# Kernel tuning notes

Hardware: AMD Instinct MI355X
Metric: run time of the kernel (lower is better)

## Reference

```python
import math
import jax, jax.numpy as jnp
import numpy as np

L, D, H, F, V, S = 4, 1024, 16, 4096, 50257, 2048
HS = D // H
EPS = 1e-5
STD = 0.02


def setup_inputs() -> dict:
    key = jax.random.key(0)
    keys = iter(jax.random.split(key, 24))

    def rn(shape):
        return (jax.random.normal(next(keys), shape, jnp.float32) * STD)

    inp = {
        "input_ids": jax.random.randint(next(keys), (1, S), 0, V, dtype=jnp.int64),
        "tok_emb": rn((V, D)),
        "pos_emb": rn((S, D)),
        # per-layer stacked params; linear weights stored [in, out]
        "Wq": rn((L, D, D)), "bq": jnp.zeros((L, D)),
        "Wk": rn((L, D, D)), "bk": jnp.zeros((L, D)),
        "Wv": rn((L, D, D)), "bv": jnp.zeros((L, D)),
        "Wo": rn((L, D, D)), "bo": jnp.zeros((L, D)),
        "W1": rn((L, D, F)), "b1": jnp.zeros((L, F)),
        "W2": rn((L, F, D)), "b2": jnp.zeros((L, D)),
        "ln1w": jnp.ones((L, D)), "ln1b": jnp.zeros((L, D)),
        "ln2w": jnp.ones((L, D)), "ln2b": jnp.zeros((L, D)),
        "lnfw": jnp.ones((D,)), "lnfb": jnp.zeros((D,)),
        "lm_head": rn((V, D)),  # torch Linear weight layout [out, in]
    }
    return inp


def _layernorm(x, w, b):
    m = jnp.mean(x, axis=-1, keepdims=True)
    v = jnp.mean(jnp.square(x - m), axis=-1, keepdims=True)
    return (x - m) * jax.lax.rsqrt(v + EPS) * w + b


def reference(input_ids, tok_emb, pos_emb, Wq, bq, Wk, bk, Wv, bv, Wo, bo,
              W1, b1, W2, b2, ln1w, ln1b, ln2w, ln2b, lnfw, lnfb, lm_head):
    B, Sq = input_ids.shape
    h = tok_emb[input_ids] + pos_emb[None, :Sq]  # [B,S,D]
    causal = jnp.tril(jnp.ones((Sq, Sq), dtype=bool))
    scale = 1.0 / math.sqrt(HS)

    def block(h, p):
        wq, bq_, wk, bk_, wv, bv_, wo, bo_, w1, b1_, w2, b2_, l1w, l1b, l2w, l2b = p
        x = _layernorm(h, l1w, l1b)
        q = (x @ wq + bq_).reshape(B, Sq, H, HS).transpose(0, 2, 1, 3)
        k = (x @ wk + bk_).reshape(B, Sq, H, HS).transpose(0, 2, 1, 3)
        v = (x @ wv + bv_).reshape(B, Sq, H, HS).transpose(0, 2, 1, 3)
        scores = jnp.einsum('bhqd,bhkd->bhqk', q, k) * scale
        scores = jnp.where(causal, scores, jnp.finfo(scores.dtype).min)
        attn = jax.nn.softmax(scores, axis=-1)  # dropout is identity at eval
        out = jnp.einsum('bhqk,bhkd->bhqd', attn, v)
        out = out.transpose(0, 2, 1, 3).reshape(B, Sq, D)
        h = h + out @ wo + bo_
        x = _layernorm(h, l2w, l2b)
        h = h + jax.nn.gelu(x @ w1 + b1_, approximate=False) @ w2 + b2_
        return h, None

    h, _ = jax.lax.scan(block, h, (Wq, bq, Wk, bk, Wv, bv, Wo, bo,
                                   W1, b1, W2, b2, ln1w, ln1b, ln2w, ln2b))
    h = _layernorm(h, lnfw, lnfb)
    logits = h @ lm_head.T  # [B,S,V]
    return logits
```

## Files before the change

kernel.cpp:

```cpp
#include <hip/hip_runtime.h>
#include <math.h>
#include <stdint.h>


#define SEQ 2048
#define DIM 1024
#define NHEAD 16
#define FFN 4096
#define VOCAB 50257
#define NLAYER 4
#define LNEPS 1e-5f
#define QKVD 3072
#define KVB 128

using bf16x8 = __attribute__((ext_vector_type(8))) short;
using s16x4  = __attribute__((ext_vector_type(4))) short;
using f32x4  = __attribute__((ext_vector_type(4))) float;
using fl4    = __attribute__((ext_vector_type(4))) float;

static __device__ __forceinline__ short f2bf(float f) {
  uint32_t u = __float_as_uint(f);
  u = (u + 0x7fffu + ((u >> 16) & 1u)) >> 16;
  return (short)u;
}
static __device__ __forceinline__ float bf2f(short s) {
  return __uint_as_float(((uint32_t)(uint16_t)s) << 16);
}
static __device__ __forceinline__ void gload_lds16(const void* g, void* l) {
  __builtin_amdgcn_global_load_lds((const __attribute__((address_space(1))) void*)g,
                                   (__attribute__((address_space(3))) void*)l, 16, 0, 0);
}

__global__ void embed_kernel(const int* __restrict__ ids,
                             const float* __restrict__ tok,
                             const float* __restrict__ pos,
                             float* __restrict__ h) {
  int i = blockIdx.x * blockDim.x + threadIdx.x;
  if (i < SEQ * DIM) {
    int s = i / DIM, d = i % DIM;
    h[i] = tok[(long)ids[s] * DIM + d] + pos[i];
  }
}

__global__ void ln_kernel(const float* __restrict__ x, const float* __restrict__ w,
                          const float* __restrict__ b, short* __restrict__ y) {
  int row = blockIdx.x;
  const float* xr = x + (long)row * DIM;
  short* yr = y + (long)row * DIM;
  int tid = threadIdx.x;
  float v0 = xr[tid], v1 = xr[tid + 256], v2 = xr[tid + 512], v3 = xr[tid + 768];
  __shared__ float red[8];
  float s = v0 + v1 + v2 + v3;
#pragma unroll
  for (int o = 32; o >= 1; o >>= 1) s += __shfl_xor(s, o);
  if ((tid & 63) == 0) red[tid >> 6] = s;
  __syncthreads();
  float mean = (red[0] + red[1] + red[2] + red[3]) * (1.f / DIM);
  float d0 = v0 - mean, d1 = v1 - mean, d2 = v2 - mean, d3 = v3 - mean;
  float q = d0 * d0 + d1 * d1 + d2 * d2 + d3 * d3;
#pragma unroll
  for (int o = 32; o >= 1; o >>= 1) q += __shfl_xor(q, o);
  if ((tid & 63) == 0) red[4 + (tid >> 6)] = q;
  __syncthreads();
  float var = (red[4] + red[5] + red[6] + red[7]) * (1.f / DIM);
  float rstd = rsqrtf(var + LNEPS);
  yr[tid]       = f2bf(d0 * rstd * w[tid] + b[tid]);
  yr[tid + 256] = f2bf(d1 * rstd * w[tid + 256] + b[tid + 256]);
  yr[tid + 512] = f2bf(d2 * rstd * w[tid + 512] + b[tid + 512]);
  yr[tid + 768] = f2bf(d3 * rstd * w[tid + 768] + b[tid + 768]);
}

__global__ void transpose_w(const float* __restrict__ in, short* __restrict__ out,
                            int K, int N) {
  __shared__ float t[32][33];
  int c0 = blockIdx.x * 32, r0 = blockIdx.y * 32;
  int tx = threadIdx.x & 31, ty = threadIdx.x >> 5;
#pragma unroll
  for (int i = 0; i < 4; i++)
    t[ty + i * 8][tx] = in[(long)(r0 + ty + i * 8) * N + c0 + tx];
  __syncthreads();
#pragma unroll
  for (int i = 0; i < 4; i++)
    out[(long)(c0 + ty + i * 8) * K + r0 + tx] = f2bf(t[tx][ty + i * 8]);
}

struct TW4 { const float* src[4]; short* dst[4]; };
__global__ void transpose_w4(TW4 p) {
  const float* in = p.src[blockIdx.z];
  short* out = p.dst[blockIdx.z];
  __shared__ float t[32][33];
  int c0 = blockIdx.x * 32, r0 = blockIdx.y * 32;
  int tx = threadIdx.x & 31, ty = threadIdx.x >> 5;
#pragma unroll
  for (int i = 0; i < 4; i++)
    t[ty + i * 8][tx] = in[(long)(r0 + ty + i * 8) * DIM + c0 + tx];
  __syncthreads();
#pragma unroll
  for (int i = 0; i < 4; i++)
    out[(long)(c0 + ty + i * 8) * DIM + r0 + tx] = f2bf(t[tx][ty + i * 8]);
}

__global__ void transpose_v(const short* __restrict__ qkv, short* __restrict__ vt) {
  __shared__ short t[64][72];
  int s0 = blockIdx.x * 64, c0 = blockIdx.y * 64;
  int tid = threadIdx.x;
#pragma unroll
  for (int i = 0; i < 2; i++) {
    int ca = i * 256 + tid;
    int row = ca >> 3, cp = ca & 7;
    bf16x8 v = *(const bf16x8*)(qkv + (long)(s0 + row) * QKVD + 2 * DIM + c0 + cp * 8);
    *(bf16x8*)&t[row][cp * 8] = v;
  }
  __syncthreads();
#pragma unroll
  for (int i = 0; i < 2; i++) {
    int ca = i * 256 + tid;
    int crow = ca >> 3, sp = ca & 7;
    s16x4 a, b;
#pragma unroll
    for (int u = 0; u < 4; u++) a[u] = t[sp * 8 + u][crow];
#pragma unroll
    for (int u = 0; u < 4; u++) b[u] = t[sp * 8 + 4 + u][crow];
    bf16x8 o;
#pragma unroll
    for (int u = 0; u < 4; u++) { o[u] = a[u]; o[4 + u] = b[u]; }
    *(bf16x8*)(vt + (long)(c0 + crow) * SEQ + s0 + sp * 8) = o;
  }
}

__global__ void conv_bf16(const float* __restrict__ in, short* __restrict__ out, long n4) {
  long i = (long)blockIdx.x * blockDim.x + threadIdx.x;
  long stride = (long)gridDim.x * blockDim.x;
  for (; i < n4; i += stride) {
    fl4 v = *(const fl4*)(in + i * 4);
    s16x4 o;
    o[0] = f2bf(v[0]); o[1] = f2bf(v[1]); o[2] = f2bf(v[2]); o[3] = f2bf(v[3]);
    *(s16x4*)(out + i * 4) = o;
  }
}

__global__ void bias_cat(const float* __restrict__ bq, const float* __restrict__ bk,
                         const float* __restrict__ bv, float* __restrict__ out) {
  int i = blockIdx.x * 256 + threadIdx.x;
  if (i < QKVD) out[i] = i < DIM ? bq[i] : (i < 2 * DIM ? bk[i - DIM] : bv[i - 2 * DIM]);
}

template <bool GELU, bool RES, bool BIAS, bool OUTBF16, int KS, bool XCDSWZ>
__global__ __launch_bounds__(256, 3) void gemm4(
    const short* __restrict__ A, const short* __restrict__ Bt,
    const float* __restrict__ bias, const float* __restrict__ res,
    void* __restrict__ Cout, int N, int Kfull) {
  __shared__ short lds[3][(128 + 128) * 32];
  const int tid = threadIdx.x, wid = tid >> 6, lane = tid & 63;
  const int l16 = lane & 15, lg = lane >> 4;
  int bx = blockIdx.x, by = blockIdx.y;
  if (XCDSWZ) {
    int gx = gridDim.x, nwg = gx * gridDim.y;
    int flat = by * gx + bx;
    int nf = (flat & 7) * (nwg >> 3) + (flat >> 3);
    bx = nf % gx; by = nf / gx;
  }
  const long m0 = (long)bx * 128, n0 = (long)by * 128;
  const int K = Kfull / KS;
  const int kbase = blockIdx.z * K;
  const int NT = K / 32;
  const int wr = (wid >> 1) * 64, wc = (wid & 1) * 64;

#define STAGE4(t, b)                                                            \
  {                                                                             \
    short* As_ = lds[b];                                                        \
    short* Bs_ = lds[b] + 128 * 32;                                             \
    int kk_ = kbase + (t) * 32;                                                 \
    _Pragma("unroll")                                                           \
    for (int i_ = 0; i_ < 2; i_++) {                                            \
      int ca_ = i_ * 256 + tid;                                                 \
      int row_ = ca_ >> 2, cp_ = ca_ & 3, c_ = cp_ ^ ((row_ >> 1) & 3);         \
      gload_lds16(A + (m0 + row_) * (long)Kfull + kk_ + c_ * 8,                 \
                  As_ + (i_ * 256 + wid * 64) * 8);                             \
    }                                                                           \
    _Pragma("unroll")                                                           \
    for (int i_ = 0; i_ < 2; i_++) {                                            \
      int ca_ = i_ * 256 + tid;                                                 \
      int row_ = ca_ >> 2, cp_ = ca_ & 3, c_ = cp_ ^ ((row_ >> 1) & 3);         \
      int rowb_ = (int)n0 + row_;                                               \
      if (rowb_ > N - 1) rowb_ = N - 1;                                         \
      gload_lds16(Bt + (long)rowb_ * Kfull + kk_ + c_ * 8,                      \
                  Bs_ + (i_ * 256 + wid * 64) * 8);                             \
    }                                                                           \
  }

  f32x4 acc[4][4] = {};
  STAGE4(0, 0);
  STAGE4(1, 1);
  asm volatile("s_waitcnt vmcnt(4)" ::: "memory");
  __builtin_amdgcn_s_barrier();
  __builtin_amdgcn_sched_barrier(0);

  for (int t = 0; t < NT; t++) {
    const int b = t % 3;
    if (t + 2 < NT) STAGE4(t + 2, (t + 2) % 3);
    const short* As = lds[b];
    const short* Bs = lds[b] + 128 * 32;
    bf16x8 af[4], bfr[4];
#pragma unroll
    for (int m = 0; m < 4; m++) {
      int row = wr + m * 16 + l16;
      af[m] = *(const bf16x8*)((const char*)As + row * 64 + ((lg ^ ((row >> 1) & 3)) * 16));
    }
#pragma unroll
    for (int n = 0; n < 4; n++) {
      int row = wc + n * 16 + l16;
      bfr[n] = *(const bf16x8*)((const char*)Bs + row * 64 + ((lg ^ ((row >> 1) & 3)) * 16));
    }
    __builtin_amdgcn_s_setprio(1);
#pragma unroll
    for (int m = 0; m < 4; m++)
#pragma unroll
      for (int n = 0; n < 4; n++)
        acc[m][n] = __builtin_amdgcn_mfma_f32_16x16x32_bf16(af[m], bfr[n], acc[m][n], 0, 0, 0);
    __builtin_amdgcn_s_setprio(0);
    if (t + 2 < NT) {
      asm volatile("s_waitcnt vmcnt(4)" ::: "memory");
    } else if (t + 1 < NT) {
      asm volatile("s_waitcnt vmcnt(0)" ::: "memory");
    }
    if (t + 1 < NT) {
      __builtin_amdgcn_s_barrier();
      __builtin_amdgcn_sched_barrier(0);
    }
  }
#undef STAGE4

  const int lr4 = lg * 4;
  if (KS == 1) {
#pragma unroll
    for (int m = 0; m < 4; m++)
#pragma unroll
      for (int n = 0; n < 4; n++)
#pragma unroll
        for (int r = 0; r < 4; r++) {
          long row = m0 + wr + m * 16 + lr4 + r;
          long col = n0 + wc + n * 16 + l16;
          if (col < N) {
            float v = acc[m][n][r];
            if (BIAS) v += bias[col];
            if (GELU) v = 0.5f * v * (1.f + erff(v * 0.70710678118f));
            if (RES) v += res[row * (long)N + col];
            if (OUTBF16) ((short*)Cout)[row * (long)N + col] = f2bf(v);
            else ((float*)Cout)[row * (long)N + col] = v;
          }
        }
  } else {
    long M = (long)gridDim.x * 128;
    float* P = (float*)Cout + (long)blockIdx.z * M * N;
#pragma unroll
    for (int m = 0; m < 4; m++)
#pragma unroll
      for (int n = 0; n < 4; n++)
#pragma unroll
        for (int r = 0; r < 4; r++) {
          long row = m0 + wr + m * 16 + lr4 + r;
          long col = n0 + wc + n * 16 + l16;
          P[row * (long)N + col] = acc[m][n][r];
        }
  }
}

template <int KS>
__global__ void reduce_k(const float* __restrict__ part, const float* __restrict__ bias,
                         float* __restrict__ h, int N, long MN) {
  long i = ((long)blockIdx.x * 256 + threadIdx.x) * 4;
  if (i >= MN) return;
  fl4 s = *(const fl4*)(h + i);
  fl4 b = *(const fl4*)(bias + (int)(i % N));
  s[0] += b[0]; s[1] += b[1]; s[2] += b[2]; s[3] += b[3];
#pragma unroll
  for (int ks = 0; ks < KS; ks++) {
    fl4 p = *(const fl4*)(part + (long)ks * MN + i);
    s[0] += p[0]; s[1] += p[1]; s[2] += p[2]; s[3] += p[3];
  }
  *(fl4*)(h + i) = s;
}

__global__ __launch_bounds__(256) void attn_mfma(const short* __restrict__ qkv,
                                                 const short* __restrict__ vtg,
                                                 short* __restrict__ Oa) {
  int hh = blockIdx.x, qb = blockIdx.y;
  int q0 = qb * 64;
  int tid = threadIdx.x, wv = tid >> 6, lane = tid & 63;
  int l16 = lane & 15, lg = lane >> 4;
  int hcol = hh * 64;
  __shared__ short Ks[KVB * 64];
  __shared__ short Vt[64 * KVB];
  __shared__ short Pl[4][16 * KVB];

  bf16x8 qf[2];
  {
    const short* qrow = qkv + (long)(q0 + wv * 16 + l16) * QKVD + hcol;
#pragma unroll
    for (int dc = 0; dc < 2; dc++) {
      bf16x8 t = *(const bf16x8*)(qrow + dc * 32 + lg * 8);
#pragma unroll
      for (int j = 0; j < 8; j++) t[j] = f2bf(bf2f(t[j]) * 0.125f);
      qf[dc] = t;
    }
  }
  f32x4 of[4] = {};
  float mrun[4], lrun[4];
#pragma unroll
  for (int r = 0; r < 4; r++) { mrun[r] = -3e38f; lrun[r] = 0.f; }

  int nt = qb / 2 + 1;
  for (int kt = 0; kt < nt; kt++) {
    int k0 = kt * KVB;
    __syncthreads();
#pragma unroll
    for (int i = 0; i < 4; i++) {
      int ca = i * 256 + tid;
      int row = ca >> 3, cp = ca & 7, c = cp ^ (row & 7);
      int ldsoff = (i * 256 + wv * 64) * 8;
      gload_lds16(qkv + (long)(k0 + row) * QKVD + DIM + hcol + c * 8, (short*)Ks + ldsoff);
    }
#pragma unroll
    for (int i = 0; i < 4; i++) {
      int ca = i * 256 + tid;
      int row = ca >> 4, cp = ca & 15, c = cp ^ (row & 7);
      int ldsoff = (i * 256 + wv * 64) * 8;
      gload_lds16(vtg + (long)(hcol + row) * SEQ + k0 + c * 8, (short*)Vt + ldsoff);
    }
    __syncthreads();

    f32x4 sacc[8] = {};
#pragma unroll
    for (int kc = 0; kc < 8; kc++) {
      int row = kc * 16 + l16;
#pragma unroll
      for (int dc = 0; dc < 2; dc++) {
        bf16x8 kf = *(const bf16x8*)((const char*)Ks + row * 128 + (((dc * 4 + lg) ^ (row & 7)) * 16));
        sacc[kc] = __builtin_amdgcn_mfma_f32_16x16x32_bf16(qf[dc], kf, sacc[kc], 0, 0, 0);
      }
    }

    float sv[8][4], pf[8][4];
#pragma unroll
    for (int kc = 0; kc < 8; kc++)
#pragma unroll
      for (int r = 0; r < 4; r++) sv[kc][r] = sacc[kc][r];
    if (kt == nt - 1) {
#pragma unroll
      for (int kc = 0; kc < 8; kc++)
#pragma unroll
        for (int r = 0; r < 4; r++) {
          int kg = k0 + kc * 16 + l16;
          int rg = q0 + wv * 16 + lg * 4 + r;
          if (kg > rg) sv[kc][r] = -3e38f;
        }
    }
    float corr[4];
#pragma unroll
    for (int r = 0; r < 4; r++) {
      float m01 = fmaxf(sv[0][r], sv[1][r]), m23 = fmaxf(sv[2][r], sv[3][r]);
      float m45 = fmaxf(sv[4][r], sv[5][r]), m67 = fmaxf(sv[6][r], sv[7][r]);
      float mt = fmaxf(fmaxf(m01, m23), fmaxf(m45, m67));
#pragma unroll
      for (int o = 8; o >= 1; o >>= 1) mt = fmaxf(mt, __shfl_xor(mt, o));
      float mn = fmaxf(mrun[r], mt);
      corr[r] = __expf(mrun[r] - mn);
      mrun[r] = mn;
      float ps = 0.f;
#pragma unroll
      for (int kc = 0; kc < 8; kc++) {
        float p = __expf(sv[kc][r] - mn);
        pf[kc][r] = p;
        ps += p;
      }
#pragma unroll
      for (int o = 8; o >= 1; o >>= 1) ps += __shfl_xor(ps, o);
      lrun[r] = lrun[r] * corr[r] + ps;
    }
#pragma unroll
    for (int c = 0; c < 4; c++)
#pragma unroll
      for (int r = 0; r < 4; r++) of[c][r] *= corr[r];
#pragma unroll
    for (int kc = 0; kc < 8; kc++)
#pragma unroll
      for (int r = 0; r < 4; r++) {
        int row = lg * 4 + r, col = kc * 16 + l16;
        int chunk = col >> 3;
        *(short*)((char*)Pl[wv] + row * 256 + ((chunk ^ (row & 7)) * 16) + (col & 7) * 2) = f2bf(pf[kc][r]);
      }
    bf16x8 pfr[4];
#pragma unroll
    for (int kc2 = 0; kc2 < 4; kc2++) {
      int cl = kc2 * 4 + lg;
      pfr[kc2] = *(const bf16x8*)((const char*)Pl[wv] + l16 * 256 + ((cl ^ (l16 & 7)) * 16));
    }
#pragma unroll
    for (int c = 0; c < 4; c++)
#pragma unroll
      for (int kc2 = 0; kc2 < 4; kc2++) {
        int vrow = c * 16 + l16;
        int cl = kc2 * 4 + lg;
        bf16x8 vf = *(const bf16x8*)((const char*)Vt + vrow * 256 + ((cl ^ (vrow & 7)) * 16));
        of[c] = __builtin_amdgcn_mfma_f32_16x16x32_bf16(pfr[kc2], vf, of[c], 0, 0, 0);
      }
  }
#pragma unroll
  for (int c = 0; c < 4; c++)
#pragma unroll
    for (int r = 0; r < 4; r++) {
      int rowg = q0 + wv * 16 + lg * 4 + r;
      int colg = hcol + c * 16 + l16;
      Oa[(long)rowg * DIM + colg] = f2bf(of[c][r] / lrun[r]);
    }
}

extern "C" void kernel_launch(void* const* d_in, const int* in_sizes, int n_in,
                              void* d_out, int out_size, void* d_ws, size_t ws_size,
                              hipStream_t stream) {
  const int* ids = (const int*)d_in[0];
  const float* tok = (const float*)d_in[1];
  const float* pos = (const float*)d_in[2];
  const float* Wq = (const float*)d_in[3];
  const float* bq = (const float*)d_in[4];
  const float* Wk = (const float*)d_in[5];
  const float* bk = (const float*)d_in[6];
  const float* Wv = (const float*)d_in[7];
  const float* bv = (const float*)d_in[8];
  const float* Wo = (const float*)d_in[9];
  const float* bo = (const float*)d_in[10];
  const float* W1 = (const float*)d_in[11];
  const float* b1 = (const float*)d_in[12];
  const float* W2 = (const float*)d_in[13];
  const float* b2 = (const float*)d_in[14];
  const float* ln1w = (const float*)d_in[15];
  const float* ln1b = (const float*)d_in[16];
  const float* ln2w = (const float*)d_in[17];
  const float* ln2b = (const float*)d_in[18];
  const float* lnfw = (const float*)d_in[19];
  const float* lnfb = (const float*)d_in[20];
  const float* lmh = (const float*)d_in[21];
  float* out = (float*)d_out;

  char* wsb = (char*)d_ws;
  float* h = (float*)wsb;
  short* x = (short*)(wsb + 8388608);
  char* big = wsb + 8388608 + 4194304;
  short* qkv  = (short*)big;
  short* a    = (short*)(big + 12582912);
  short* vt   = (short*)(big + 16777216);
  short* fbuf = (short*)(big + 20971520);
  float* pproj = (float*)fbuf;
  float* pffn2 = (float*)big;
  char* wdyn = big + 37748736;
  short* wqkvT = (short*)wdyn;
  short* woT   = (short*)(wdyn + 6291456);
  short* w1T   = (short*)(wdyn + 8388608);
  short* w2T   = (short*)(wdyn + 16777216);
  float* bias3 = (float*)(wdyn + 25165824);
  short* lmhB = (short*)big;

  const long MN = (long)SEQ * DIM;

  embed_kernel<<<(SEQ * DIM + 255) / 256, 256, 0, stream>>>(ids, tok, pos, h);

  dim3 gQKV(SEQ / 128, QKVD / 128);
  dim3 gPROJ(SEQ / 128, DIM / 128, 2);
  dim3 gFFN1(SEQ / 128, FFN / 128);
  dim3 gFFN2(SEQ / 128, DIM / 128, 2);
  dim3 gV(SEQ / 128, (VOCAB + 127) / 128);

  for (int l = 0; l < NLAYER; l++) {
    TW4 tw;
    tw.src[0] = Wq + (long)l * DIM * DIM; tw.dst[0] = wqkvT;
    tw.src[1] = Wk + (long)l * DIM * DIM; tw.dst[1] = wqkvT + (long)DIM * DIM;
    tw.src[2] = Wv + (long)l * DIM * DIM; tw.dst[2] = wqkvT + (long)2 * DIM * DIM;
    tw.src[3] = Wo + (long)l * DIM * DIM; tw.dst[3] = woT;
    transpose_w4<<<dim3(32, 32, 4), 256, 0, stream>>>(tw);
    transpose_w<<<dim3(128, 32), 256, 0, stream>>>(W1 + (long)l * DIM * FFN, w1T, DIM, FFN);
    transpose_w<<<dim3(32, 128), 256, 0, stream>>>(W2 + (long)l * FFN * DIM, w2T, FFN, DIM);
    bias_cat<<<12, 256, 0, stream>>>(bq + (long)l * DIM, bk + (long)l * DIM, bv + (long)l * DIM, bias3);

    ln_kernel<<<SEQ, 256, 0, stream>>>(h, ln1w + (long)l * DIM, ln1b + (long)l * DIM, x);
    gemm4<false, false, true, true, 1, true><<<gQKV, 256, 0, stream>>>(x, wqkvT, bias3, nullptr, qkv, QKVD, DIM);
    transpose_v<<<dim3(SEQ / 64, DIM / 64), 256, 0, stream>>>(qkv, vt);
    attn_mfma<<<dim3(NHEAD, SEQ / 64), 256, 0, stream>>>(qkv, vt, a);
    gemm4<false, false, false, false, 2, true><<<gPROJ, 256, 0, stream>>>(a, woT, nullptr, nullptr, pproj, DIM, DIM);
    reduce_k<2><<<(int)(MN / 1024), 256, 0, stream>>>(pproj, bo + (long)l * DIM, h, DIM, MN);
    ln_kernel<<<SEQ, 256, 0, stream>>>(h, ln2w + (long)l * DIM, ln2b + (long)l * DIM, x);
    gemm4<true, false, true, true, 1, true><<<gFFN1, 256, 0, stream>>>(x, w1T, b1 + (long)l * FFN, nullptr, fbuf, FFN, DIM);
    gemm4<false, false, false, false, 2, true><<<gFFN2, 256, 0, stream>>>(fbuf, w2T, nullptr, nullptr, pffn2, DIM, FFN);
    reduce_k<2><<<(int)(MN / 1024), 256, 0, stream>>>(pffn2, b2 + (long)l * DIM, h, DIM, MN);
  }

  ln_kernel<<<SEQ, 256, 0, stream>>>(h, lnfw, lnfb, x);
  conv_bf16<<<2048, 256, 0, stream>>>(lmh, lmhB, (long)VOCAB * DIM / 4);
  gemm4<false, false, false, false, 1, true><<<gV, 256, 0, stream>>>(x, lmhB, nullptr, nullptr, out, VOCAB, DIM);
}
```

Measured before the change: 1.151 ms.

## Add 256x256 tiled 8-wave GEMM with phased LDS pipeline for LM head

Introduces a new GEMM kernel with 256x256 output tiles, 512 threads, 64-wide K steps, double-buffered swizzled LDS and interleaved async loads and MFMA phases with priority hints. It replaces the 128x128 gemm4 for the vocabulary projection. The larger tile is meant to cut global and LDS traffic per FLOP and improve MFMA utilisation on the largest GEMM. The trade-offs are heavier register and LDS use, which lowers occupancy, and fewer workgroups (8x197), which may tail-balance worse across CUs. The fused XCD swizzle requires the workgroup count to be divisible by 8, which 8x197 satisfies.

Result: no change. 1.150 ms (-0.2%).

```diff
diff --git a/kernel.cpp b/kernel.cpp
--- a/kernel.cpp
+++ b/kernel.cpp
@@ -143,6 +143,129 @@
                          const float* __restrict__ bv, float* __restrict__ out) {
   int i = blockIdx.x * 256 + threadIdx.x;
   if (i < QKVD) out[i] = i < DIM ? bq[i] : (i < 2 * DIM ? bk[i - DIM] : bv[i - 2 * DIM]);
+}
+
+template <bool XCDSWZ>
+__global__ __launch_bounds__(512, 2) void gemm256(
+    const short* __restrict__ A, const short* __restrict__ Bt,
+    float* __restrict__ C, int N, int K) {
+  __shared__ short ldsA[2][256 * 64];
+  __shared__ short ldsB[2][256 * 64];
+  const int tid = threadIdx.x, wid = tid >> 6, lane = tid & 63;
+  const int l16 = lane & 15, lg = lane >> 4;
+  const int wm = wid >> 2, wn = wid & 3;
+  int bx = blockIdx.x, by = blockIdx.y;
+  if (XCDSWZ) {
+    int gx = gridDim.x, nwg = gx * gridDim.y;
+    int flat = by * gx + bx;
+    int nf = (flat & 7) * (nwg >> 3) + (flat >> 3);
+    bx = nf % gx; by = nf / gx;
+  }
+  const long m0 = (long)bx * 256, n0 = (long)by * 256;
+  const int NT = K / 64;
+
+  auto SA = [&](int t, int b, int r0) {
+    int row = r0 + wid * 8 + (lane >> 3);
+    int c = (lane & 7) ^ (row & 7);
+    gload_lds16(A + (m0 + row) * (long)K + t * 64 + c * 8,
+                &ldsA[b][(r0 + wid * 8) * 64]);
+  };
+  auto SB = [&](int t, int b, int r0) {
+    int row = r0 + wid * 8 + (lane >> 3);
+    int c = (lane & 7) ^ (row & 7);
+    int rowb = (int)n0 + row;
+    if (rowb > N - 1) rowb = N - 1;
+    gload_lds16(Bt + (long)rowb * K + t * 64 + c * 8,
+                &ldsB[b][(r0 + wid * 8) * 64]);
+  };
+
+  f32x4 acc[8][4] = {};
+  bf16x8 bfr[4][2];
+
+  auto PH = [&](int b, int q) {
+    bf16x8 af[2][2];
+    if (q == 0) {
+#pragma unroll
+      for (int nf = 0; nf < 4; nf++) {
+        int row = wn * 64 + nf * 16 + l16;
+#pragma unroll
+        for (int ks = 0; ks < 2; ks++)
+          bfr[nf][ks] = *(const bf16x8*)((const char*)&ldsB[b][0] + row * 128 +
+                                         (((ks * 4 + lg) ^ (row & 7)) * 16));
+      }
+    }
+#pragma unroll
+    for (int j = 0; j < 2; j++) {
+      int row = wm * 128 + (q * 2 + j) * 16 + l16;
+#pragma unroll
+      for (int ks = 0; ks < 2; ks++)
+        af[j][ks] = *(const bf16x8*)((const char*)&ldsA[b][0] + row * 128 +
+                                     (((ks * 4 + lg) ^ (row & 7)) * 16));
+    }
+    __builtin_amdgcn_s_barrier();
+    __builtin_amdgcn_s_setprio(1);
+#pragma unroll
+    for (int ks = 0; ks < 2; ks++)
+#pragma unroll
+      for (int j = 0; j < 2; j++)
+#pragma unroll
+        for (int nf = 0; nf < 4; nf++)
+          acc[q * 2 + j][nf] =
+              __builtin_amdgcn_mfma_f32_16x16x32_bf16(af[j][ks], bfr[nf][ks],
+                                                      acc[q * 2 + j][nf], 0, 0, 0);
+    __builtin_amdgcn_s_setprio(0);
+  };
+
+  SA(0, 0, 0); SA(0, 0, 64); SA(0, 0, 128); SA(0, 0, 192);
+  SB(0, 0, 0); SB(0, 0, 64); SB(0, 0, 128); SB(0, 0, 192);
+  SA(1, 1, 0); SA(1, 1, 128);
+  asm volatile("s_waitcnt vmcnt(2)" ::: "memory");
+  __builtin_amdgcn_s_barrier();
+
+  for (int i = 0; i < NT / 2; i++) {
+    const int e = 2 * i, o = e + 1;
+    const bool more = (e + 2) < NT;
+    SA(o, 1, 64); SA(o, 1, 192);
+    PH(0, 0);
+    __builtin_amdgcn_s_barrier();
+    SB(o, 1, 0); SB(o, 1, 64);
+    PH(0, 1);
+    __builtin_amdgcn_s_barrier();
+    SB(o, 1, 128); SB(o, 1, 192);
+    PH(0, 2);
+    __builtin_amdgcn_s_barrier();
+    if (more) { SA(e + 2, 0, 0); SA(e + 2, 0, 128); }
+    PH(0, 3);
+    if (more) asm volatile("s_waitcnt vmcnt(2)" ::: "memory");
+    else      asm volatile("s_waitcnt vmcnt(0)" ::: "memory");
+    __builtin_amdgcn_s_barrier();
+    if (more) { SA(e + 2, 0, 64); SA(e + 2, 0, 192); }
+    PH(1, 0);
+    __builtin_amdgcn_s_barrier();
+    if (more) { SB(e + 2, 0, 0); SB(e + 2, 0, 64); }
+    PH(1, 1);
+    __builtin_amdgcn_s_barrier();
+    if (more) { SB(e + 2, 0, 128); SB(e + 2, 0, 192); }
+    PH(1, 2);
+    __builtin_amdgcn_s_barrier();
+    if (more) { SA(e + 3, 1, 0); SA(e + 3, 1, 128); }
+    PH(1, 3);
+    if (more) {
+      asm volatile("s_waitcnt vmcnt(2)" ::: "memory");
+      __builtin_amdgcn_s_barrier();
+    }
+  }
+
+#pragma unroll
+  for (int mf = 0; mf < 8; mf++)
+#pragma unroll
+    for (int nf = 0; nf < 4; nf++)
+#pragma unroll
+      for (int r = 0; r < 4; r++) {
+        long row = m0 + wm * 128 + mf * 16 + lg * 4 + r;
+        long col = n0 + wn * 64 + nf * 16 + l16;
+        if (col < N) C[row * (long)N + col] = acc[mf][nf][r];
+      }
 }
 
 template <bool GELU, bool RES, bool BIAS, bool OUTBF16, int KS, bool XCDSWZ>
@@ -469,7 +592,7 @@
   dim3 gPROJ(SEQ / 128, DIM / 128, 2);
   dim3 gFFN1(SEQ / 128, FFN / 128);
   dim3 gFFN2(SEQ / 128, DIM / 128, 2);
-  dim3 gV(SEQ / 128, (VOCAB + 127) / 128);
+  dim3 gV(SEQ / 256, (VOCAB + 255) / 256);
 
   for (int l = 0; l < NLAYER; l++) {
     TW4 tw;
@@ -496,5 +619,5 @@
 
   ln_kernel<<<SEQ, 256, 0, stream>>>(h, lnfw, lnfb, x);
   conv_bf16<<<2048, 256, 0, stream>>>(lmh, lmhB, (long)VOCAB * DIM / 4);
-  gemm4<false, false, false, false, 1, true><<<gV, 256, 0, stream>>>(x, lmhB, nullptr, nullptr, out, VOCAB, DIM);
-}
+  gemm256<true><<<gV, 512, 0, stream>>>(x, lmhB, out, VOCAB, DIM);
+}
```
